# Optimization experiments

Measured on AMD Instinct MI355X. Metric: run time of the kernel, lower is better.

Reference implementation:

```python
import jax, jax.numpy as jnp
import numpy as np

B, S, DM, H = 4, 4096, 1024, 16
HD = DM // H

def setup_inputs() -> dict:
    key = jax.random.key(0)
    ks = jax.random.split(key, 9)
    sc = 1.0 / np.sqrt(DM)
    return {
        "x": jax.random.normal(ks[0], (B, S, DM), dtype=jnp.float32),
        "Wq": jax.random.normal(ks[1], (DM, DM), dtype=jnp.float32) * sc,
        "bq": jnp.zeros((DM,), dtype=jnp.float32),
        "Wk": jax.random.normal(ks[2], (DM, DM), dtype=jnp.float32) * sc,
        "bk": jnp.zeros((DM,), dtype=jnp.float32),
        "Wv": jax.random.normal(ks[3], (DM, DM), dtype=jnp.float32) * sc,
        "bv": jnp.zeros((DM,), dtype=jnp.float32),
        "Wo": jax.random.normal(ks[4], (DM, DM), dtype=jnp.float32) * sc,
        "bo": jnp.zeros((DM,), dtype=jnp.float32),
    }

def _heads(t):
    # [B,S,DM] -> [B,H,S,HD]
    return t.reshape(B, S, H, HD).transpose(0, 2, 1, 3)

def reference(x, Wq, bq, Wk, bk, Wv, bv, Wo, bo):
    q = _heads(x @ Wq.T + bq)
    k = _heads(x @ Wk.T + bk)
    v = _heads(x @ Wv.T + bv)
    q = jax.nn.elu(q) + 1.0  # positive feature map
    k = jax.nn.elu(k) + 1.0
    # kv aggregation: [B,H,HD,HD]
    kv = jnp.einsum('bhsd,bhse->bhde', k, v)
    qkv = jnp.einsum('bhsd,bhde->bhse', q, kv)  # [B,H,S,HD]
    k_sum = k.sum(axis=2)  # [B,H,HD]
    normalizer = jnp.einsum('bhsd,bhd->bhs', q, k_sum) + 1e-6
    out = qkv / normalizer[..., None]
    out = out.transpose(0, 2, 1, 3).reshape(B, S, DM)
    return out @ Wo.T + bo  # dropout is identity in eval
```

## Files before the change

### kernel.cpp

```cpp
#include <hip/hip_runtime.h>
#include <math.h>

#define NROWS  16384
#define DMODEL 1024
#define NHEAD  16
#define HDIM   64
#define SEQ    4096
#define NBATCH 4
#define NBH    64
#define SCHUNK 16
#define W1     2097152u

typedef __attribute__((ext_vector_type(8))) short bf16x8;
typedef __attribute__((ext_vector_type(4))) float f32x4;

#define VMCNT(N) asm volatile("s_waitcnt vmcnt(" #N ")" ::: "memory")
#define BAR() do { asm volatile("" ::: "memory"); __builtin_amdgcn_s_barrier(); \
                   asm volatile("" ::: "memory"); } while (0)

__device__ __forceinline__ unsigned short f2bf(float f) {
    unsigned u = __float_as_uint(f);
    u += 0x7FFFu + ((u >> 16) & 1u);
    return (unsigned short)(u >> 16);
}
__device__ __forceinline__ float bf2f(unsigned short h) {
    return __uint_as_float((unsigned)h << 16);
}

__device__ __forceinline__ void gload16(const void* g, void* l) {
    __builtin_amdgcn_global_load_lds(
        (const __attribute__((address_space(1))) unsigned int*)g,
        (__attribute__((address_space(3))) unsigned int*)l, 16, 0, 0);
}

__global__ __launch_bounds__(256)
void split_x(const float* __restrict__ a, unsigned short* __restrict__ dst)
{
    const int idx = blockIdx.x * 256 + threadIdx.x;
    const int row = idx >> 8;
    const int c4  = (idx & 255) * 4;
    const float4 v = ((const float4*)a)[idx];
    ushort4 H, L;
    H.x = f2bf(v.x); L.x = f2bf(v.x - bf2f(H.x));
    H.y = f2bf(v.y); L.y = f2bf(v.y - bf2f(H.y));
    H.z = f2bf(v.z); L.z = f2bf(v.z - bf2f(H.z));
    H.w = f2bf(v.w); L.w = f2bf(v.w - bf2f(H.w));
    *(ushort4*)&dst[(size_t)row * 2048 + c4]        = H;
    *(ushort4*)&dst[(size_t)row * 2048 + 1024 + c4] = L;
}

__global__ __launch_bounds__(256)
void split_w4(const float* __restrict__ a0, const float* __restrict__ a1,
              const float* __restrict__ a2, const float* __restrict__ a3,
              unsigned short* __restrict__ dst)
{
    const int y = blockIdx.y;
    const float* src = (y == 0) ? a0 : (y == 1) ? a1 : (y == 2) ? a2 : a3;
    unsigned short* d = dst + (size_t)y * W1;
    const int idx = blockIdx.x * 256 + threadIdx.x;
    const int row = idx >> 8;
    const int c4  = (idx & 255) * 4;
    const float4 v = ((const float4*)src)[idx];
    ushort4 H, L;
    H.x = f2bf(v.x); L.x = f2bf(v.x - bf2f(H.x));
    H.y = f2bf(v.y); L.y = f2bf(v.y - bf2f(H.y));
    H.z = f2bf(v.z); L.z = f2bf(v.z - bf2f(H.z));
    H.w = f2bf(v.w); L.w = f2bf(v.w - bf2f(H.w));
    *(ushort4*)&d[(size_t)row * 2048 + c4]        = H;
    *(ushort4*)&d[(size_t)row * 2048 + 1024 + c4] = L;
}

template<int ELU>
__global__ __launch_bounds__(512)
void gemm_p3(const unsigned short* __restrict__ A2, const unsigned short* __restrict__ W2,
             const float* __restrict__ bias, float* __restrict__ C)
{
    __shared__ unsigned short lds[65536];
    const int t    = threadIdx.x;
    const int lane = t & 63;
    const int wv   = t >> 6;
    const int wr   = wv >> 2;
    const int wcn  = wv & 3;

    const int bid  = blockIdx.x;
    const int swz  = ((bid & 7) << 5) | (bid >> 3);
    const int am0  = (swz >> 2) * 256;
    const int bn0  = (swz & 3) * 256;

    const int fr   = lane & 15;
    const int j0   = lane >> 4;
    const unsigned fro = (unsigned)(j0 * 128 + fr * 8);
    const int srcr = lane & 15;
    const int srcc = (lane >> 4) * 8;

    f32x4 acc[8][4];
#pragma unroll
    for (int i = 0; i < 8; ++i)
#pragma unroll
        for (int j = 0; j < 4; ++j)
#pragma unroll
            for (int e = 0; e < 4; ++e) acc[i][j][e] = 0.f;

    auto stage_tile = [&](int kt) {
        const int k0  = kt * 32;
        const int kbA = (k0 < 1024) ? k0 : k0 - 1024;
        const int kbB = (k0 < 2048) ? k0 : k0 - 2048;
        const unsigned wb = ((unsigned)kt & 3u) * 16384u;
#pragma unroll
        for (int c = 0; c < 2; ++c) {
            const int ch = wv * 2 + c;
            gload16(A2 + (size_t)(am0 + ch * 16 + srcr) * 2048 + kbA + srcc,
                    (unsigned short*)&lds[wb + (unsigned)ch * 512u]);
            gload16(W2 + (size_t)(bn0 + ch * 16 + srcr) * 2048 + kbB + srcc,
                    (unsigned short*)&lds[wb + 8192u + (unsigned)ch * 512u]);
        }
    };

    auto compute = [&](int kt) {
        const unsigned rd = ((unsigned)kt & 3u) * 16384u;
        bf16x8 a[8], b[4];
#pragma unroll
        for (int j = 0; j < 4; ++j)
            b[j] = *(const bf16x8*)&lds[rd + 8192u + (unsigned)((wcn * 4 + j) * 512) + fro];
#pragma unroll
        for (int i = 0; i < 8; ++i)
            a[i] = *(const bf16x8*)&lds[rd + (unsigned)((wr * 8 + i) * 512) + fro];
        __builtin_amdgcn_s_setprio(1);
#pragma unroll
        for (int i = 0; i < 8; ++i)
#pragma unroll
            for (int j = 0; j < 4; ++j)
                acc[i][j] = __builtin_amdgcn_mfma_f32_16x16x32_bf16(a[i], b[j], acc[i][j], 0, 0, 0);
        __builtin_amdgcn_s_setprio(0);
    };

    stage_tile(0); stage_tile(1); stage_tile(2);

    for (int kt = 0; kt < 93; ++kt) {
        VMCNT(8);
        BAR();
        stage_tile(kt + 3);
        compute(kt);
    }
    VMCNT(8); BAR(); compute(93);
    VMCNT(4); BAR(); compute(94);
    VMCNT(0); BAR(); compute(95);

    const int crow0 = am0 + wr * 128 + (lane >> 4) * 4;
    const int ccol0 = bn0 + wcn * 64 + fr;
#pragma unroll
    for (int j = 0; j < 4; ++j) {
        const int col = ccol0 + j * 16;
        const float bv = bias[col];
#pragma unroll
        for (int i = 0; i < 8; ++i) {
            const int row = crow0 + i * 16;
#pragma unroll
            for (int r = 0; r < 4; ++r) {
                float v = acc[i][j][r] + bv;
                if (ELU) v = (v > 0.f) ? (v + 1.f) : __expf(v);
                C[(size_t)(row + r) * DMODEL + col] = v;
            }
        }
    }
}

__global__ __launch_bounds__(512)
void kv_partial(const float* __restrict__ k, const float* __restrict__ v,
                float* __restrict__ kvp, float* __restrict__ ksp)
{
    __shared__ float Ks[32][64];
    __shared__ float Vs[32][64];
    const int t  = threadIdx.x;
    const int bh = blockIdx.x;
    const int b  = bh >> 4;
    const int h  = bh & 15;
    const int sc = blockIdx.y;
    const int d  = t & 63;
    const int e0 = (t >> 6) * 8;

    float acc[8];
#pragma unroll
    for (int j = 0; j < 8; ++j) acc[j] = 0.f;
    float ks = 0.f;

    const size_t rowbase = (size_t)b * SEQ;
    const int sbeg = sc * (SEQ / SCHUNK);
    const int send = sbeg + (SEQ / SCHUNK);
    const int lrow = t >> 4;
    const int lc4  = (t & 15) * 4;

    for (int s0 = sbeg; s0 < send; s0 += 32) {
        const size_t g = (rowbase + s0 + lrow) * DMODEL + h * HDIM + lc4;
        *(float4*)&Ks[lrow][lc4] = *(const float4*)&k[g];
        *(float4*)&Vs[lrow][lc4] = *(const float4*)&v[g];
        __syncthreads();
#pragma unroll 8
        for (int sp = 0; sp < 32; ++sp) {
            const float kd = Ks[sp][d];
            if (t < 64) ks += Ks[sp][t];
            const float4 v0 = *(const float4*)&Vs[sp][e0 + 0];
            const float4 v1 = *(const float4*)&Vs[sp][e0 + 4];
            acc[0] = fmaf(kd, v0.x, acc[0]);  acc[1] = fmaf(kd, v0.y, acc[1]);
            acc[2] = fmaf(kd, v0.z, acc[2]);  acc[3] = fmaf(kd, v0.w, acc[3]);
            acc[4] = fmaf(kd, v1.x, acc[4]);  acc[5] = fmaf(kd, v1.y, acc[5]);
            acc[6] = fmaf(kd, v1.z, acc[6]);  acc[7] = fmaf(kd, v1.w, acc[7]);
        }
        __syncthreads();
    }

    const size_t base = ((size_t)sc * NBH + bh) * HDIM;
    float4 o0; o0.x = acc[0]; o0.y = acc[1]; o0.z = acc[2]; o0.w = acc[3];
    float4 o1; o1.x = acc[4]; o1.y = acc[5]; o1.z = acc[6]; o1.w = acc[7];
    *(float4*)&kvp[(base + d) * HDIM + e0 + 0] = o0;
    *(float4*)&kvp[(base + d) * HDIM + e0 + 4] = o1;
    if (t < 64) ksp[base + t] = ks;
}

__global__ __launch_bounds__(256)
void kv_reduce(const float* __restrict__ kvp, const float* __restrict__ ksp,
               float* __restrict__ kv, float* __restrict__ ksum)
{
    const int i = blockIdx.x * 256 + threadIdx.x;
    const int NKV = NBH * HDIM * HDIM;
    if (i < NKV) {
        float s = 0.f;
#pragma unroll
        for (int c = 0; c < SCHUNK; ++c) s += kvp[(size_t)c * NKV + i];
        kv[i] = s;
    }
    if (i < NBH * HDIM) {
        float s = 0.f;
#pragma unroll
        for (int c = 0; c < SCHUNK; ++c) s += ksp[(size_t)c * NBH * HDIM + i];
        ksum[i] = s;
    }
}

__global__ __launch_bounds__(256)
void qkv_norm(const float* __restrict__ q, const float* __restrict__ kv,
              const float* __restrict__ ksum, unsigned short* __restrict__ att)
{
    __shared__ float Qs[64][68];
    __shared__ float KVs[64][64];
    __shared__ float kss[64];
    const int t  = threadIdx.x;
    const int s0 = blockIdx.x * 64;
    const int b  = blockIdx.y;
    const int h  = blockIdx.z;
    const int bh = b * NHEAD + h;

#pragma unroll
    for (int i = 0; i < 4; ++i) {
        const int idx = i * 256 + t;
        const int row = idx >> 4;
        const int c4  = (idx & 15) * 4;
        const float4 vq = *(const float4*)&q[((size_t)b * SEQ + s0 + row) * DMODEL + h * HDIM + c4];
        *(float4*)&Qs[row][c4] = vq;
        *(float4*)&((float*)KVs)[idx * 4] = *(const float4*)&kv[(size_t)bh * HDIM * HDIM + idx * 4];
    }
    if (t < 64) kss[t] = ksum[(size_t)bh * HDIM + t];
    __syncthreads();

    const int r  = t >> 2;
    const int e0 = (t & 3) * 16;
    float out[16];
#pragma unroll
    for (int j = 0; j < 16; ++j) out[j] = 0.f;
    float nrm = 0.f;

#pragma unroll 8
    for (int d = 0; d < 64; ++d) {
        const float qd = Qs[r][d];
        nrm = fmaf(qd, kss[d], nrm);
        const float4 k0 = *(const float4*)&KVs[d][e0 + 0];
        const float4 k1 = *(const float4*)&KVs[d][e0 + 4];
        const float4 k2 = *(const float4*)&KVs[d][e0 + 8];
        const float4 k3 = *(const float4*)&KVs[d][e0 + 12];
        out[0]  = fmaf(qd, k0.x, out[0]);  out[1]  = fmaf(qd, k0.y, out[1]);
        out[2]  = fmaf(qd, k0.z, out[2]);  out[3]  = fmaf(qd, k0.w, out[3]);
        out[4]  = fmaf(qd, k1.x, out[4]);  out[5]  = fmaf(qd, k1.y, out[5]);
        out[6]  = fmaf(qd, k1.z, out[6]);  out[7]  = fmaf(qd, k1.w, out[7]);
        out[8]  = fmaf(qd, k2.x, out[8]);  out[9]  = fmaf(qd, k2.y, out[9]);
        out[10] = fmaf(qd, k2.z, out[10]); out[11] = fmaf(qd, k2.w, out[11]);
        out[12] = fmaf(qd, k3.x, out[12]); out[13] = fmaf(qd, k3.y, out[13]);
        out[14] = fmaf(qd, k3.z, out[14]); out[15] = fmaf(qd, k3.w, out[15]);
    }

    const float inv = 1.f / (nrm + 1e-6f);
    const size_t gb = ((size_t)b * SEQ + s0 + r) * 2048 + h * HDIM + e0;
#pragma unroll
    for (int g4 = 0; g4 < 4; ++g4) {
        ushort4 H, L;
        const float v0 = out[g4*4+0] * inv;
        const float v1 = out[g4*4+1] * inv;
        const float v2 = out[g4*4+2] * inv;
        const float v3 = out[g4*4+3] * inv;
        H.x = f2bf(v0); L.x = f2bf(v0 - bf2f(H.x));
        H.y = f2bf(v1); L.y = f2bf(v1 - bf2f(H.y));
        H.z = f2bf(v2); L.z = f2bf(v2 - bf2f(H.z));
        H.w = f2bf(v3); L.w = f2bf(v3 - bf2f(H.w));
        *(ushort4*)&att[gb + g4 * 4]        = H;
        *(ushort4*)&att[gb + 1024 + g4 * 4] = L;
    }
}

extern "C" void kernel_launch(void* const* d_in, const int* in_sizes, int n_in,
                              void* d_out, int out_size, void* d_ws, size_t ws_size,
                              hipStream_t stream)
{
    const float* x  = (const float*)d_in[0];
    const float* Wq = (const float*)d_in[1];
    const float* bq = (const float*)d_in[2];
    const float* Wk = (const float*)d_in[3];
    const float* bk = (const float*)d_in[4];
    const float* Wv = (const float*)d_in[5];
    const float* bv = (const float*)d_in[6];
    const float* Wo = (const float*)d_in[7];
    const float* bo = (const float*)d_in[8];

    unsigned short* xs  = (unsigned short*)d_ws;
    unsigned short* wsp = xs + (size_t)NROWS * 2048;
    float* buf0 = (float*)(wsp + 4u * W1);
    float* kv   = buf0 + (size_t)NROWS * DMODEL;
    float* ksum = kv + NBH * HDIM * HDIM;
    float* kvp  = ksum + NBH * HDIM;
    float* ksp  = kvp + (size_t)SCHUNK * NBH * HDIM * HDIM;
    float* vbuf = (float*)d_out;

    const dim3 gg(256);

    split_w4<<<dim3(1024, 4), 256, 0, stream>>>(Wq, Wk, Wv, Wo, wsp);
    split_x<<<16384, 256, 0, stream>>>(x, xs);
    gemm_p3<1><<<gg, 512, 0, stream>>>(xs, wsp + 1u * W1, bk, buf0);
    gemm_p3<0><<<gg, 512, 0, stream>>>(xs, wsp + 2u * W1, bv, vbuf);
    kv_partial<<<dim3(NBH, SCHUNK), 512, 0, stream>>>(buf0, vbuf, kvp, ksp);
    kv_reduce<<<1024, 256, 0, stream>>>(kvp, ksp, kv, ksum);
    gemm_p3<1><<<gg, 512, 0, stream>>>(xs, wsp, bq, buf0);
    qkv_norm<<<dim3(SEQ / 64, NBATCH, NHEAD), 256, 0, stream>>>(buf0, kv, ksum, xs);
    gemm_p3<0><<<gg, 512, 0, stream>>>(xs, wsp + 3u * W1, bo, (float*)d_out);
}
```

Measured before the change: 560.9 us.

## Restructure GEMM main loop into double-buffered 64-wide K tiles with four interleaved phases

The GEMM K loop moves from a 4-stage ring of 32-wide tiles to two 64-wide buffers. Each tile is processed in four phases that each read half the A fragments, issue one slot of global-to-LDS loads for the next tile, and run 16 MFMAs, with a barrier around every phase. The intent is to interleave loads, LDS reads and MFMA work more finely and to spread memory traffic across the tile. In exchange the pipeline is shallower (one tile of prefetch instead of three) and there are more barriers per K step.

```diff
diff --git a/kernel.cpp b/kernel.cpp
--- a/kernel.cpp
+++ b/kernel.cpp
@@ -72,7 +72,7 @@
 
 template<int ELU>
 __global__ __launch_bounds__(512)
-void gemm_p3(const unsigned short* __restrict__ A2, const unsigned short* __restrict__ W2,
+void gemm_8p(const unsigned short* __restrict__ A2, const unsigned short* __restrict__ W2,
              const float* __restrict__ bias, float* __restrict__ C)
 {
     __shared__ unsigned short lds[65536];
@@ -89,7 +89,7 @@
 
     const int fr   = lane & 15;
     const int j0   = lane >> 4;
-    const unsigned fro = (unsigned)(j0 * 128 + fr * 8);
+    const unsigned fro = (unsigned)((j0 * 16 + fr) * 8);
     const int srcr = lane & 15;
     const int srcc = (lane >> 4) * 8;
 
@@ -101,50 +101,67 @@
 #pragma unroll
             for (int e = 0; e < 4; ++e) acc[i][j][e] = 0.f;
 
-    auto stage_tile = [&](int kt) {
-        const int k0  = kt * 32;
-        const int kbA = (k0 < 1024) ? k0 : k0 - 1024;
-        const int kbB = (k0 < 2048) ? k0 : k0 - 2048;
-        const unsigned wb = ((unsigned)kt & 3u) * 16384u;
+    auto stage_slot = [&](int kt, int sl) {
+        const int  kh  = sl >> 1;
+        const bool isA = ((sl & 1) == 0);
+        const int  k0  = kt * 64 + kh * 32;
+        const int  kb  = isA ? ((k0 < 1024) ? k0 : k0 - 1024)
+                             : ((k0 < 2048) ? k0 : k0 - 2048);
+        const unsigned short* src = isA ? A2 : W2;
+        const int  rb  = isA ? am0 : bn0;
+        const unsigned slb = ((unsigned)kt & 1u) * 32768u
+                           + (isA ? 0u : 16384u) + (unsigned)kh * 8192u;
 #pragma unroll
         for (int c = 0; c < 2; ++c) {
             const int ch = wv * 2 + c;
-            gload16(A2 + (size_t)(am0 + ch * 16 + srcr) * 2048 + kbA + srcc,
-                    (unsigned short*)&lds[wb + (unsigned)ch * 512u]);
-            gload16(W2 + (size_t)(bn0 + ch * 16 + srcr) * 2048 + kbB + srcc,
-                    (unsigned short*)&lds[wb + 8192u + (unsigned)ch * 512u]);
+            gload16(src + (size_t)(rb + ch * 16 + srcr) * 2048 + kb + srcc,
+                    (unsigned short*)&lds[slb + (unsigned)ch * 512u]);
         }
     };
 
-    auto compute = [&](int kt) {
-        const unsigned rd = ((unsigned)kt & 3u) * 16384u;
-        bf16x8 a[8], b[4];
-#pragma unroll
-        for (int j = 0; j < 4; ++j)
-            b[j] = *(const bf16x8*)&lds[rd + 8192u + (unsigned)((wcn * 4 + j) * 512) + fro];
-#pragma unroll
-        for (int i = 0; i < 8; ++i)
-            a[i] = *(const bf16x8*)&lds[rd + (unsigned)((wr * 8 + i) * 512) + fro];
+    bf16x8 bfr[4];
+
+    auto phase = [&](int kt, int ph, int ktn) {
+        const unsigned bb = ((unsigned)kt & 1u) * 32768u;
+        const int kh = ph >> 1;
+        const int rg = (ph & 1) * 4;
+        if ((ph & 1) == 0) {
+#pragma unroll
+            for (int j = 0; j < 4; ++j)
+                bfr[j] = *(const bf16x8*)&lds[bb + 16384u + (unsigned)kh * 8192u
+                                              + (unsigned)((wcn * 4 + j) * 512) + fro];
+        }
+        bf16x8 afr[4];
+#pragma unroll
+        for (int i = 0; i < 4; ++i)
+            afr[i] = *(const bf16x8*)&lds[bb + (unsigned)kh * 8192u
+                                          + (unsigned)((wr * 8 + rg + i) * 512) + fro];
+        if (ktn >= 0) stage_slot(ktn, ph);
+        BAR();
         __builtin_amdgcn_s_setprio(1);
 #pragma unroll
-        for (int i = 0; i < 8; ++i)
+        for (int i = 0; i < 4; ++i)
 #pragma unroll
             for (int j = 0; j < 4; ++j)
-                acc[i][j] = __builtin_amdgcn_mfma_f32_16x16x32_bf16(a[i], b[j], acc[i][j], 0, 0, 0);
+                acc[rg + i][j] = __builtin_amdgcn_mfma_f32_16x16x32_bf16(
+                    afr[i], bfr[j], acc[rg + i][j], 0, 0, 0);
         __builtin_amdgcn_s_setprio(0);
     };
 
-    stage_tile(0); stage_tile(1); stage_tile(2);
-
-    for (int kt = 0; kt < 93; ++kt) {
-        VMCNT(8);
-        BAR();
-        stage_tile(kt + 3);
-        compute(kt);
-    }
-    VMCNT(8); BAR(); compute(93);
-    VMCNT(4); BAR(); compute(94);
-    VMCNT(0); BAR(); compute(95);
+    stage_slot(0, 0); stage_slot(0, 1); stage_slot(0, 2); stage_slot(0, 3);
+    VMCNT(4);
+    BAR();
+
+    for (int kt = 0; kt < 47; ++kt) {
+        phase(kt, 0, kt + 1); BAR();
+        phase(kt, 1, kt + 1); VMCNT(4); BAR();
+        phase(kt, 2, kt + 1); BAR();
+        phase(kt, 3, kt + 1); VMCNT(4); BAR();
+    }
+    phase(47, 0, -1); BAR();
+    phase(47, 1, -1); VMCNT(0); BAR();
+    phase(47, 2, -1); BAR();
+    phase(47, 3, -1);
 
     const int crow0 = am0 + wr * 128 + (lane >> 4) * 4;
     const int ccol0 = bn0 + wcn * 64 + fr;
@@ -332,11 +349,11 @@
 
     split_w4<<<dim3(1024, 4), 256, 0, stream>>>(Wq, Wk, Wv, Wo, wsp);
     split_x<<<16384, 256, 0, stream>>>(x, xs);
-    gemm_p3<1><<<gg, 512, 0, stream>>>(xs, wsp + 1u * W1, bk, buf0);
-    gemm_p3<0><<<gg, 512, 0, stream>>>(xs, wsp + 2u * W1, bv, vbuf);
+    gemm_8p<1><<<gg, 512, 0, stream>>>(xs, wsp + 1u * W1, bk, buf0);
+    gemm_8p<0><<<gg, 512, 0, stream>>>(xs, wsp + 2u * W1, bv, vbuf);
     kv_partial<<<dim3(NBH, SCHUNK), 512, 0, stream>>>(buf0, vbuf, kvp, ksp);
     kv_reduce<<<1024, 256, 0, stream>>>(kvp, ksp, kv, ksum);
-    gemm_p3<1><<<gg, 512, 0, stream>>>(xs, wsp, bq, buf0);
+    gemm_8p<1><<<gg, 512, 0, stream>>>(xs, wsp, bq, buf0);
     qkv_norm<<<dim3(SEQ / 64, NBATCH, NHEAD), 256, 0, stream>>>(buf0, kv, ksum, xs);
-    gemm_p3<0><<<gg, 512, 0, stream>>>(xs, wsp + 3u * W1, bo, (float*)d_out);
-}
+    gemm_8p<0><<<gg, 512, 0, stream>>>(xs, wsp + 3u * W1, bo, (float*)d_out);
+}
```

Result: no change. 564.4 us (+0.6%).
